# Performance work log

Measured on AMD Instinct MI355X. Metric: run time of the kernel, lower is better.

## Reference

```python
import jax, jax.numpy as jnp
import numpy as np

MIN_CURV = 1e-06
MIN_NORM = 1e-15

def _norm(x):
    return jnp.clip(jnp.linalg.norm(x, axis=-1, keepdims=True), MIN_NORM, None)

def lorentz_expmap0(v, c):
    sqrt_c = jnp.sqrt(c)
    vn = _norm(v)
    x0 = jnp.cosh(sqrt_c * vn) / sqrt_c
    xs = jnp.sinh(sqrt_c * vn) * v / (sqrt_c * vn)
    return jnp.concatenate([x0, xs], axis=-1)

def lorentz_logmap0(x, c):
    sqrt_c = jnp.sqrt(c)
    x0 = x[..., 0:1]
    xs = x[..., 1:]
    xs_norm = _norm(xs)
    theta = jnp.arccosh(jnp.clip(sqrt_c * x0, 1.0 + 1e-07, None))
    return theta / (sqrt_c * xs_norm) * xs

def lorentz_project(x, c):
    spatial = x[..., 1:]
    sq = jnp.sum(spatial * spatial, axis=-1, keepdims=True)
    x0 = jnp.clip(jnp.sqrt(sq + 1.0 / c), MIN_NORM, None)
    return jnp.concatenate([x0, spatial], axis=-1)

def givens_rotation(x, angles):
    x0 = x[..., 0:1]
    xs = x[..., 1:]
    cos_a = jnp.cos(angles)
    sin_a = jnp.sin(angles)
    xe = xs[..., 0::2]
    xo = xs[..., 1::2]
    ne = cos_a * xe - sin_a * xo
    no = sin_a * xe + cos_a * xo
    xr = jnp.stack([ne, no], axis=-1).reshape(xs.shape)
    return jnp.concatenate([x0, xr], axis=-1)

def setup_inputs() -> dict:
    key = jax.random.key(0)
    ks = jax.random.split(key, 16)
    N_NODE, E, B = 50000, 500000, 64
    IN_DIM, OUT_DIM, ATTN_DIM, N_REL = 128, 128, 128, 200
    N_EMB = 2 * N_REL + 1  # 401
    hidden = jax.random.normal(ks[0], (N_NODE, IN_DIM), dtype=jnp.float32)
    q_sub = jax.random.randint(ks[1], (B,), 0, N_NODE)
    q_rel = jax.random.randint(ks[2], (B,), 0, N_EMB)
    r_idx = jax.random.randint(ks[3], (E,), 0, B)
    rel = jax.random.randint(ks[4], (E,), 0, N_EMB)
    sub = jax.random.randint(ks[5], (E,), 0, N_NODE)
    obj = jax.random.randint(ks[6], (E,), 0, N_NODE)
    zeros = jnp.zeros((E,), dtype=jnp.int32)
    edges = jnp.stack([r_idx, zeros, rel, zeros, sub, obj], axis=1)
    rela_embed = jax.random.normal(ks[7], (N_EMB, IN_DIM), dtype=jnp.float32)
    rel_angles = jax.random.uniform(ks[8], (N_EMB, IN_DIM // 2), minval=-0.1, maxval=0.1, dtype=jnp.float32)
    curvature = jnp.array(1.0, dtype=jnp.float32)
    Ws_w = jax.random.normal(ks[9], (ATTN_DIM, IN_DIM), dtype=jnp.float32) * 0.05
    Wr_w = jax.random.normal(ks[10], (ATTN_DIM, IN_DIM), dtype=jnp.float32) * 0.05
    Wqr_w = jax.random.normal(ks[11], (ATTN_DIM, IN_DIM), dtype=jnp.float32) * 0.05
    Wqr_b = jax.random.normal(ks[12], (ATTN_DIM,), dtype=jnp.float32) * 0.05
    Wattn_w = jax.random.normal(ks[13], (1, ATTN_DIM), dtype=jnp.float32) * 0.05
    Wh_w = jax.random.normal(ks[14], (OUT_DIM, IN_DIM), dtype=jnp.float32) * 0.05
    return {"hidden": hidden, "rela_embed": rela_embed, "rel_angles": rel_angles,
            "curvature": curvature, "Ws_w": Ws_w, "Wr_w": Wr_w, "Wqr_w": Wqr_w,
            "Wqr_b": Wqr_b, "Wattn_w": Wattn_w, "Wh_w": Wh_w,
            "q_sub": q_sub, "q_rel": q_rel, "edges": edges,
            "n_node": N_NODE, "old_nodes_new_idx": jnp.arange(N_NODE)}

def reference(hidden, rela_embed, rel_angles, curvature, Ws_w, Wr_w, Wqr_w, Wqr_b,
              Wattn_w, Wh_w, q_sub, q_rel, edges, n_node, old_nodes_new_idx):
    sub = edges[:, 4]
    rel = edges[:, 2]
    obj = edges[:, 5]
    r_idx = edges[:, 0]
    hs = hidden[sub]                      # [E, in_dim]
    hr = rela_embed[rel]                  # [E, in_dim]
    h_qr = rela_embed[q_rel][r_idx]       # [E, in_dim]
    pre = jax.nn.relu(hs @ Ws_w.T + hr @ Wr_w.T + h_qr @ Wqr_w.T + Wqr_b)
    alpha = jax.nn.sigmoid(pre @ Wattn_w.T)  # [E, 1]
    c = jnp.clip(curvature, MIN_CURV, None)
    mess_tangent = hs + hr
    mess_L = lorentz_expmap0(mess_tangent, c)          # [E, in_dim+1]
    mess_L = givens_rotation(mess_L, rel_angles[rel])
    mess2 = lorentz_logmap0(mess_L, c)                 # [E, in_dim]
    message = mess2 * alpha
    message_agg = jax.ops.segment_sum(message, obj, num_segments=n_node)
    a = message_agg @ Wh_w.T                           # [n_node, out_dim]
    a_L = lorentz_expmap0(a, c)
    # act is identity; project back to hyperboloid and log-map
    a_L = lorentz_project(jnp.concatenate([a_L[..., 0:1], a_L[..., 1:]], axis=-1), c)
    hidden_new = lorentz_logmap0(a_L, c)
    return hidden_new
```

## Files before the change

kernel.cpp:

```cpp
#include <hip/hip_runtime.h>
#include <math.h>

#define D 128
#define CAP 36

typedef _Float16 f16x8 __attribute__((ext_vector_type(8)));
typedef _Float16 f16x4 __attribute__((ext_vector_type(4)));
typedef _Float16 f16x2 __attribute__((ext_vector_type(2)));
typedef float    f32x4 __attribute__((ext_vector_type(4)));

union H8 { f16x8 v; f16x4 q[2]; f16x2 p[4]; _Float16 f[8]; };
union H4 { f16x4 v; f16x2 p[2]; _Float16 f[4]; };

__device__ __forceinline__ float fdot2f(f16x2 a, f16x2 b, float c){
  return __builtin_amdgcn_fdot2(a, b, c, false);
}
__device__ __forceinline__ f16x2 relu2(f16x2 x){
  f16x2 r;
  r[0] = x[0] > (_Float16)0 ? x[0] : (_Float16)0;
  r[1] = x[1] > (_Float16)0 ? x[1] : (_Float16)0;
  return r;
}
__device__ __forceinline__ float rsum32(float v){
  v += __shfl_xor(v, 16);
  v += __shfl_xor(v, 8);
  v += __shfl_xor(v, 4);
  v += __shfl_xor(v, 2);
  v += __shfl_xor(v, 1);
  return v;
}

__global__ void k_cvt_small(const float* __restrict__ rela,
                            const float* __restrict__ rel_angles,
                            const float* __restrict__ Ws, const float* __restrict__ Wr,
                            const float* __restrict__ Wh,
                            _Float16* __restrict__ rela16, _Float16* __restrict__ relhq,
                            _Float16* __restrict__ relcs, _Float16* __restrict__ Ws16,
                            _Float16* __restrict__ Wr16, _Float16* __restrict__ Wh16,
                            int* __restrict__ cnt, int NEMB, int NN){
  int idx = blockIdx.x*blockDim.x + threadIdx.x;
  int T1 = NEMB*32;
  if (idx < T1){
    int r = idx >> 5, l = idx & 31;
    float4 hv = *(const float4*)(rela + (size_t)r*D + l*4);
    f16x4 h = { (_Float16)hv.x, (_Float16)hv.y, (_Float16)hv.z, (_Float16)hv.w };
    *(f16x4*)(rela16 + (size_t)r*D + l*4) = h;
    *(f16x4*)(relhq  + (size_t)r*256 + l*8) = h;
    float2 an = *(const float2*)(rel_angles + (size_t)r*(D/2) + l*2);
    float c0 = cosf(an.x), s0 = sinf(an.x);
    float c1 = cosf(an.y), s1 = sinf(an.y);
    H8 cs;
    cs.f[0]=(_Float16)c0; cs.f[1]=(_Float16)(-s0); cs.f[2]=(_Float16)s0; cs.f[3]=(_Float16)c0;
    cs.f[4]=(_Float16)c1; cs.f[5]=(_Float16)(-s1); cs.f[6]=(_Float16)s1; cs.f[7]=(_Float16)c1;
    *(f16x8*)(relcs + (size_t)r*256 + l*8) = cs.v;
    return;
  }
  int j = idx - T1;
  if (j < 3*D*D/4){
    const float* src = (j < 4096) ? Ws : (j < 8192) ? Wr : Wh;
    _Float16*    dst = (j < 4096) ? Ws16 : (j < 8192) ? Wr16 : Wh16;
    int o = (j & 4095)*4;
    float4 v = *(const float4*)(src + o);
    f16x4 h = { (_Float16)v.x, (_Float16)v.y, (_Float16)v.z, (_Float16)v.w };
    *(f16x4*)(dst + o) = h;
    return;
  }
  j -= 3*D*D/4;
  if (j < NN) cnt[j] = 0;
}

__global__ __launch_bounds__(128) void k_prep2(const float* __restrict__ rela,
                                               const float* __restrict__ Wqr,
                                               const float* __restrict__ Wqr_b,
                                               const int* __restrict__ q_rel,
                                               _Float16* __restrict__ hqw16){
  int b = blockIdx.x; int t = threadIdx.x;
  __shared__ float emb[D];
  emb[t] = rela[(size_t)q_rel[b]*D + t];
  __syncthreads();
  float acc = Wqr_b[t];
  #pragma unroll 8
  for (int k=0;k<D;k++) acc += emb[k]*Wqr[t*D + k];
  int p = ((t & 15) << 3) + (t >> 4);
  hqw16[b*D + p] = (_Float16)acc;
}

template<int OUTMODE>
__global__ __launch_bounds__(256) void k_hgemm(const _Float16* __restrict__ A,
                                               const _Float16* __restrict__ W,
                                               void* __restrict__ Out, int M){
  int wave = threadIdx.x >> 6;
  int lane = threadIdx.x & 63;
  int quad = lane >> 4;
  int lo   = lane & 15;
  int m0 = blockIdx.x*64 + wave*16;
  int arow = min(m0 + lo, M-1);
  f32x4 acc[8];
  #pragma unroll
  for (int nt=0;nt<8;nt++) acc[nt] = (f32x4){0.f,0.f,0.f,0.f};
  #pragma unroll
  for (int kt=0;kt<4;kt++){
    f16x8 a = *(const f16x8*)(A + (size_t)arow*D + kt*32 + quad*8);
    #pragma unroll
    for (int nt=0;nt<8;nt++){
      f16x8 b = *(const f16x8*)(W + (size_t)(nt*16 + lo)*D + kt*32 + quad*8);
      acc[nt] = __builtin_amdgcn_mfma_f32_16x16x32_f16(a, b, acc[nt], 0, 0, 0);
    }
  }
  int r0 = m0 + quad*4;
  if (OUTMODE == 0){
    float* O = (float*)Out;
    #pragma unroll
    for (int nt=0;nt<8;nt++){
      int c = nt*16 + lo;
      #pragma unroll
      for (int i=0;i<4;i++){
        int r = r0 + i;
        if (r < M) O[(size_t)r*D + c] = acc[nt][i];
      }
    }
  } else {
    _Float16* O = (_Float16*)Out;
    #pragma unroll
    for (int i=0;i<4;i++){
      int r = r0 + i;
      if (r < M){
        H4 s1, s2;
        #pragma unroll
        for (int nt=0;nt<4;nt++){
          s1.f[nt] = (_Float16)acc[nt][i];
          s2.f[nt] = (_Float16)acc[nt+4][i];
        }
        *(f16x4*)(O + (size_t)r*256 + lo*16 + 4)  = s1.v;
        *(f16x4*)(O + (size_t)r*256 + lo*16 + 12) = s2.v;
      }
    }
  }
}

__global__ __launch_bounds__(256) void k_hgemm_h(const float* __restrict__ A,
                                                 const _Float16* __restrict__ W,
                                                 _Float16* __restrict__ O, int M){
  int wave = threadIdx.x >> 6;
  int lane = threadIdx.x & 63;
  int quad = lane >> 4;
  int lo   = lane & 15;
  int m0 = blockIdx.x*64 + wave*16;
  int arow = min(m0 + lo, M-1);
  f32x4 acc[8];
  #pragma unroll
  for (int nt=0;nt<8;nt++) acc[nt] = (f32x4){0.f,0.f,0.f,0.f};
  H8 hpack[4];
  #pragma unroll
  for (int kt=0;kt<4;kt++){
    float4 a0 = *(const float4*)(A + (size_t)arow*D + kt*32 + quad*8);
    float4 a1 = *(const float4*)(A + (size_t)arow*D + kt*32 + quad*8 + 4);
    H8 a;
    a.f[0]=(_Float16)a0.x; a.f[1]=(_Float16)a0.y; a.f[2]=(_Float16)a0.z; a.f[3]=(_Float16)a0.w;
    a.f[4]=(_Float16)a1.x; a.f[5]=(_Float16)a1.y; a.f[6]=(_Float16)a1.z; a.f[7]=(_Float16)a1.w;
    hpack[kt] = a;
    #pragma unroll
    for (int nt=0;nt<8;nt++){
      f16x8 b = *(const f16x8*)(W + (size_t)(nt*16 + lo)*D + kt*32 + quad*8);
      acc[nt] = __builtin_amdgcn_mfma_f32_16x16x32_f16(a.v, b, acc[nt], 0, 0, 0);
    }
  }
  if (m0 + lo < M){
    #pragma unroll
    for (int kt=0;kt<4;kt++){
      int g = kt*8 + quad*2;
      *(f16x4*)(O + (size_t)arow*256 + g*8)     = hpack[kt].q[0];
      *(f16x4*)(O + (size_t)arow*256 + (g+1)*8) = hpack[kt].q[1];
    }
  }
  int r0 = m0 + quad*4;
  #pragma unroll
  for (int i=0;i<4;i++){
    int r = r0 + i;
    if (r < M){
      H4 s1, s2;
      #pragma unroll
      for (int nt=0;nt<4;nt++){
        s1.f[nt] = (_Float16)acc[nt][i];
        s2.f[nt] = (_Float16)acc[nt+4][i];
      }
      *(f16x4*)(O + (size_t)r*256 + lo*16 + 4)  = s1.v;
      *(f16x4*)(O + (size_t)r*256 + lo*16 + 12) = s2.v;
    }
  }
}

__global__ void k_scatter(const int* __restrict__ edges, int* __restrict__ cnt,
                          int* __restrict__ bucket, int E){
  int base = (blockIdx.x*blockDim.x + threadIdx.x)*2;
  #pragma unroll
  for (int u=0; u<2; u++){
    int e = base + u;
    if (e < E){
      const int* er = edges + (size_t)e*6;
      int ri = er[0], rel = er[2], sub = er[4], obj = er[5];
      int key = sub | (rel << 17) | (ri << 26);
      int pos = atomicAdd(cnt + obj, 1);
      if (pos < CAP) bucket[obj*CAP + pos] = key;
    }
  }
}

__device__ __forceinline__ void edge_op(int key,
    const _Float16* __restrict__ hw16, const _Float16* __restrict__ relcs,
    const _Float16* __restrict__ relhq, const _Float16* __restrict__ hqw16,
    unsigned lh8, unsigned lh4, f16x2 wa01, f16x2 wa23,
    float& ax, float& ay, float& az, float& aw){
  unsigned sub = key & 0x1FFFF, rel = ((unsigned)key >> 17) & 0x1FF, ri = (unsigned)key >> 26;
  H8 hw; hw.v = *(const f16x8*)(hw16  + (sub << 8) + lh8);
  H8 cs; cs.v = *(const f16x8*)(relcs + (rel << 8) + lh8);
  H8 hq; hq.v = *(const f16x8*)(relhq + (rel << 8) + lh8);
  H4 qw; qw.v = *(const f16x4*)(hqw16 + (ri  << 7) + lh4);
  f16x2 t01 = relu2(hw.p[2] + hq.p[2] + qw.p[0]);
  f16x2 t23 = relu2(hw.p[3] + hq.p[3] + qw.p[1]);
  float s = fdot2f(t01, wa01, fdot2f(t23, wa23, 0.f));
  s = rsum32(s);
  float al = __builtin_amdgcn_rcpf(1.f + __expf(-s));
  f16x2 v01 = hw.p[0] + hq.p[0];
  f16x2 v23 = hw.p[1] + hq.p[1];
  ax += al * fdot2f(cs.p[0], v01, 0.f);
  ay += al * fdot2f(cs.p[1], v01, 0.f);
  az += al * fdot2f(cs.p[2], v23, 0.f);
  aw += al * fdot2f(cs.p[3], v23, 0.f);
}

__global__ __launch_bounds__(256) void k_aggregate(
    const _Float16* __restrict__ hw16, const _Float16* __restrict__ relcs,
    const _Float16* __restrict__ relhq, const _Float16* __restrict__ hqw16,
    const float* __restrict__ Wattn, const int* __restrict__ cnt,
    const int* __restrict__ bucket, _Float16* __restrict__ agg16, int NN){
  int t = threadIdx.x;
  int wave = t >> 6;
  int half = (t >> 5) & 1;
  int l = t & 31;
  int n = blockIdx.x*4 + wave;
  if (n >= NN) return;
  unsigned lh8 = (unsigned)l*8, lh4 = (unsigned)l*4;
  unsigned p0 = (unsigned)l*4;
  float w0 = Wattn[(((p0+0)&7)<<4) + ((p0+0)>>3)];
  float w1 = Wattn[(((p0+1)&7)<<4) + ((p0+1)>>3)];
  float w2 = Wattn[(((p0+2)&7)<<4) + ((p0+2)>>3)];
  float w3 = Wattn[(((p0+3)&7)<<4) + ((p0+3)>>3)];
  f16x2 wa01 = { (_Float16)w0, (_Float16)w1 };
  f16x2 wa23 = { (_Float16)w2, (_Float16)w3 };

  int deg = min(cnt[n], CAP);
  const int* bk = bucket + n*CAP;
  float ax=0.f, ay=0.f, az=0.f, aw=0.f;

  for (int i = half*4; i < deg; i += 8){
    int m = deg - i;
    if (m >= 4){
      int4 q = *(const int4*)(bk + i);
      edge_op(q.x, hw16, relcs, relhq, hqw16, lh8, lh4, wa01, wa23, ax, ay, az, aw);
      edge_op(q.y, hw16, relcs, relhq, hqw16, lh8, lh4, wa01, wa23, ax, ay, az, aw);
      edge_op(q.z, hw16, relcs, relhq, hqw16, lh8, lh4, wa01, wa23, ax, ay, az, aw);
      edge_op(q.w, hw16, relcs, relhq, hqw16, lh8, lh4, wa01, wa23, ax, ay, az, aw);
    } else {
      for (int j=0;j<m;j++)
        edge_op(bk[i+j], hw16, relcs, relhq, hqw16, lh8, lh4, wa01, wa23, ax, ay, az, aw);
    }
  }
  ax += __shfl_xor(ax, 32);
  ay += __shfl_xor(ay, 32);
  az += __shfl_xor(az, 32);
  aw += __shfl_xor(aw, 32);
  if (half == 0){
    f16x4 o = { (_Float16)ax, (_Float16)ay, (_Float16)az, (_Float16)aw };
    *(f16x4*)(agg16 + ((size_t)n << 7) + lh4) = o;
  }
}

extern "C" void kernel_launch(void* const* d_in, const int* in_sizes, int n_in,
                              void* d_out, int out_size, void* d_ws, size_t ws_size,
                              hipStream_t stream){
  const float* hidden     = (const float*)d_in[0];
  const float* rela       = (const float*)d_in[1];
  const float* rel_angles = (const float*)d_in[2];
  const float* Ws         = (const float*)d_in[4];
  const float* Wr         = (const float*)d_in[5];
  const float* Wqr        = (const float*)d_in[6];
  const float* Wqr_b      = (const float*)d_in[7];
  const float* Wattn      = (const float*)d_in[8];
  const float* Wh         = (const float*)d_in[9];
  const int*   q_rel      = (const int*)d_in[11];
  const int*   edges      = (const int*)d_in[12];

  int NN   = in_sizes[0] / D;
  int NEMB = in_sizes[1] / D;
  int B    = in_sizes[11];
  int E    = in_sizes[12] / 6;

  char* p = (char*)d_ws;
  auto alloc = [&](size_t bytes)->char*{
    char* r = p; p += (bytes + 255) & ~(size_t)255; return r;
  };
  _Float16* hw16   = (_Float16*)alloc((size_t)NN*256*2);
  _Float16* agg16  = (_Float16*)alloc((size_t)NN*D*2);
  _Float16* rela16 = (_Float16*)alloc((size_t)NEMB*D*2);
  _Float16* relhq  = (_Float16*)alloc((size_t)NEMB*256*2);
  _Float16* relcs  = (_Float16*)alloc((size_t)NEMB*256*2);
  _Float16* hqw16  = (_Float16*)alloc((size_t)B*D*2);
  _Float16* Ws16   = (_Float16*)alloc((size_t)D*D*2);
  _Float16* Wr16   = (_Float16*)alloc((size_t)D*D*2);
  _Float16* Wh16   = (_Float16*)alloc((size_t)D*D*2);
  int*      cnt    = (int*)alloc((size_t)NN*4);
  int*      bucket = (int*)alloc((size_t)NN*CAP*4);

  int smallN = NEMB*32 + 3*D*D/4 + NN;
  k_cvt_small<<<(smallN+255)/256, 256, 0, stream>>>(rela, rel_angles, Ws, Wr, Wh,
                                                    rela16, relhq, relcs,
                                                    Ws16, Wr16, Wh16, cnt, NEMB, NN);
  k_prep2<<<B, 128, 0, stream>>>(rela, Wqr, Wqr_b, q_rel, hqw16);
  k_hgemm<1><<<(NEMB+63)/64, 256, 0, stream>>>(rela16, Wr16, relhq, NEMB);
  k_hgemm_h<<<(NN+63)/64, 256, 0, stream>>>(hidden, Ws16, hw16, NN);
  k_scatter<<<(E/2+255)/256, 256, 0, stream>>>(edges, cnt, bucket, E);
  k_aggregate<<<(NN+3)/4, 256, 0, stream>>>(hw16, relcs, relhq, hqw16,
                                            Wattn, cnt, bucket, agg16, NN);
  k_hgemm<0><<<(NN+63)/64, 256, 0, stream>>>(agg16, Wh16, d_out, NN);
}
```

Baseline: 259.3 us.

## Remap aggregate to 8 edges per wave with wider per-lane feature tiles

The aggregate kernel now has each wave process 8 edges at once, with 8 lanes per edge and each lane covering 16 features. Previously it walked edges sequentially with 32 lanes per edge. To match, the packed fp16 tables (relhq, relcs, hw16, hqw16) are relaid so each lane reads contiguous 32-element chunks with 16-byte loads, and the GEMM epilogues write 16-byte vectors. The attention reduction drops from a 5-step shuffle to 3 steps, in exchange for a 48-shuffle final cross-group reduction and more registers per lane. The scatter kernel also reads edge rows as int4 vectors.

After: 270.7 us. 1.04x slower.

```diff
diff --git a/kernel.cpp b/kernel.cpp
--- a/kernel.cpp
+++ b/kernel.cpp
@@ -10,7 +10,7 @@
 typedef float    f32x4 __attribute__((ext_vector_type(4)));
 
 union H8 { f16x8 v; f16x4 q[2]; f16x2 p[4]; _Float16 f[8]; };
-union H4 { f16x4 v; f16x2 p[2]; _Float16 f[4]; };
+
 
 __device__ __forceinline__ float fdot2f(f16x2 a, f16x2 b, float c){
   return __builtin_amdgcn_fdot2(a, b, c, false);
@@ -20,14 +20,6 @@
   r[0] = x[0] > (_Float16)0 ? x[0] : (_Float16)0;
   r[1] = x[1] > (_Float16)0 ? x[1] : (_Float16)0;
   return r;
-}
-__device__ __forceinline__ float rsum32(float v){
-  v += __shfl_xor(v, 16);
-  v += __shfl_xor(v, 8);
-  v += __shfl_xor(v, 4);
-  v += __shfl_xor(v, 2);
-  v += __shfl_xor(v, 1);
-  return v;
 }
 
 __global__ void k_cvt_small(const float* __restrict__ rela,
@@ -45,14 +37,14 @@
     float4 hv = *(const float4*)(rela + (size_t)r*D + l*4);
     f16x4 h = { (_Float16)hv.x, (_Float16)hv.y, (_Float16)hv.z, (_Float16)hv.w };
     *(f16x4*)(rela16 + (size_t)r*D + l*4) = h;
-    *(f16x4*)(relhq  + (size_t)r*256 + l*8) = h;
+    *(f16x4*)(relhq + (size_t)r*256 + (l>>2)*32 + (l&3)*4) = h;
     float2 an = *(const float2*)(rel_angles + (size_t)r*(D/2) + l*2);
     float c0 = cosf(an.x), s0 = sinf(an.x);
     float c1 = cosf(an.y), s1 = sinf(an.y);
     H8 cs;
     cs.f[0]=(_Float16)c0; cs.f[1]=(_Float16)(-s0); cs.f[2]=(_Float16)s0; cs.f[3]=(_Float16)c0;
     cs.f[4]=(_Float16)c1; cs.f[5]=(_Float16)(-s1); cs.f[6]=(_Float16)s1; cs.f[7]=(_Float16)c1;
-    *(f16x8*)(relcs + (size_t)r*256 + l*8) = cs.v;
+    *(f16x8*)(relcs + (size_t)r*256 + (l>>2)*32 + (l&3)*8) = cs.v;
     return;
   }
   int j = idx - T1;
@@ -81,7 +73,7 @@
   float acc = Wqr_b[t];
   #pragma unroll 8
   for (int k=0;k<D;k++) acc += emb[k]*Wqr[t*D + k];
-  int p = ((t & 15) << 3) + (t >> 4);
+  int p = (t&7)*16 + (t&8) + (t>>4);
   hqw16[b*D + p] = (_Float16)acc;
 }
 
@@ -121,18 +113,15 @@
     }
   } else {
     _Float16* O = (_Float16*)Out;
+    int wbase = (lo&7)*32 + 16 + (lo&8);
     #pragma unroll
     for (int i=0;i<4;i++){
       int r = r0 + i;
       if (r < M){
-        H4 s1, s2;
+        H8 s;
         #pragma unroll
-        for (int nt=0;nt<4;nt++){
-          s1.f[nt] = (_Float16)acc[nt][i];
-          s2.f[nt] = (_Float16)acc[nt+4][i];
-        }
-        *(f16x4*)(O + (size_t)r*256 + lo*16 + 4)  = s1.v;
-        *(f16x4*)(O + (size_t)r*256 + lo*16 + 12) = s2.v;
+        for (int nt=0;nt<8;nt++) s.f[nt] = (_Float16)acc[nt][i];
+        *(f16x8*)(O + (size_t)r*256 + wbase) = s.v;
       }
     }
   }
@@ -168,65 +157,40 @@
   if (m0 + lo < M){
     #pragma unroll
     for (int kt=0;kt<4;kt++){
-      int g = kt*8 + quad*2;
-      *(f16x4*)(O + (size_t)arow*256 + g*8)     = hpack[kt].q[0];
-      *(f16x4*)(O + (size_t)arow*256 + (g+1)*8) = hpack[kt].q[1];
+      int base = (kt*2 + (quad>>1))*32 + (quad&1)*8;
+      *(f16x8*)(O + (size_t)arow*256 + base) = hpack[kt].v;
     }
   }
   int r0 = m0 + quad*4;
+  int wbase = (lo&7)*32 + 16 + (lo&8);
   #pragma unroll
   for (int i=0;i<4;i++){
     int r = r0 + i;
     if (r < M){
-      H4 s1, s2;
+      H8 s;
       #pragma unroll
-      for (int nt=0;nt<4;nt++){
-        s1.f[nt] = (_Float16)acc[nt][i];
-        s2.f[nt] = (_Float16)acc[nt+4][i];
-      }
-      *(f16x4*)(O + (size_t)r*256 + lo*16 + 4)  = s1.v;
-      *(f16x4*)(O + (size_t)r*256 + lo*16 + 12) = s2.v;
+      for (int nt=0;nt<8;nt++) s.f[nt] = (_Float16)acc[nt][i];
+      *(f16x8*)(O + (size_t)r*256 + wbase) = s.v;
     }
   }
 }
 
 __global__ void k_scatter(const int* __restrict__ edges, int* __restrict__ cnt,
                           int* __restrict__ bucket, int E){
-  int base = (blockIdx.x*blockDim.x + threadIdx.x)*2;
-  #pragma unroll
-  for (int u=0; u<2; u++){
-    int e = base + u;
-    if (e < E){
-      const int* er = edges + (size_t)e*6;
-      int ri = er[0], rel = er[2], sub = er[4], obj = er[5];
-      int key = sub | (rel << 17) | (ri << 26);
-      int pos = atomicAdd(cnt + obj, 1);
-      if (pos < CAP) bucket[obj*CAP + pos] = key;
-    }
-  }
-}
-
-__device__ __forceinline__ void edge_op(int key,
-    const _Float16* __restrict__ hw16, const _Float16* __restrict__ relcs,
-    const _Float16* __restrict__ relhq, const _Float16* __restrict__ hqw16,
-    unsigned lh8, unsigned lh4, f16x2 wa01, f16x2 wa23,
-    float& ax, float& ay, float& az, float& aw){
-  unsigned sub = key & 0x1FFFF, rel = ((unsigned)key >> 17) & 0x1FF, ri = (unsigned)key >> 26;
-  H8 hw; hw.v = *(const f16x8*)(hw16  + (sub << 8) + lh8);
-  H8 cs; cs.v = *(const f16x8*)(relcs + (rel << 8) + lh8);
-  H8 hq; hq.v = *(const f16x8*)(relhq + (rel << 8) + lh8);
-  H4 qw; qw.v = *(const f16x4*)(hqw16 + (ri  << 7) + lh4);
-  f16x2 t01 = relu2(hw.p[2] + hq.p[2] + qw.p[0]);
-  f16x2 t23 = relu2(hw.p[3] + hq.p[3] + qw.p[1]);
-  float s = fdot2f(t01, wa01, fdot2f(t23, wa23, 0.f));
-  s = rsum32(s);
-  float al = __builtin_amdgcn_rcpf(1.f + __expf(-s));
-  f16x2 v01 = hw.p[0] + hq.p[0];
-  f16x2 v23 = hw.p[1] + hq.p[1];
-  ax += al * fdot2f(cs.p[0], v01, 0.f);
-  ay += al * fdot2f(cs.p[1], v01, 0.f);
-  az += al * fdot2f(cs.p[2], v23, 0.f);
-  aw += al * fdot2f(cs.p[3], v23, 0.f);
+  int e0 = (blockIdx.x*blockDim.x + threadIdx.x)*2;
+  if (e0 >= E) return;
+  const int4* q = (const int4*)(edges + (size_t)e0*6);
+  int4 q0 = q[0], q1 = q[1], q2 = q[2];
+  {
+    int key = q1.x | (q0.z << 17) | (q0.x << 26);
+    int pos = atomicAdd(cnt + q1.y, 1);
+    if (pos < CAP) bucket[q1.y*CAP + pos] = key;
+  }
+  if (e0 + 1 < E){
+    int key = q2.z | (q2.x << 17) | (q1.z << 26);
+    int pos = atomicAdd(cnt + q2.w, 1);
+    if (pos < CAP) bucket[q2.w*CAP + pos] = key;
+  }
 }
 
 __global__ __launch_bounds__(256) void k_aggregate(
@@ -235,44 +199,80 @@
     const float* __restrict__ Wattn, const int* __restrict__ cnt,
     const int* __restrict__ bucket, _Float16* __restrict__ agg16, int NN){
   int t = threadIdx.x;
-  int wave = t >> 6;
-  int half = (t >> 5) & 1;
-  int l = t & 31;
+  int wave = t >> 6, lane = t & 63;
+  int g = lane >> 3, j = lane & 7;
   int n = blockIdx.x*4 + wave;
   if (n >= NN) return;
-  unsigned lh8 = (unsigned)l*8, lh4 = (unsigned)l*4;
-  unsigned p0 = (unsigned)l*4;
-  float w0 = Wattn[(((p0+0)&7)<<4) + ((p0+0)>>3)];
-  float w1 = Wattn[(((p0+1)&7)<<4) + ((p0+1)>>3)];
-  float w2 = Wattn[(((p0+2)&7)<<4) + ((p0+2)>>3)];
-  float w3 = Wattn[(((p0+3)&7)<<4) + ((p0+3)>>3)];
-  f16x2 wa01 = { (_Float16)w0, (_Float16)w1 };
-  f16x2 wa23 = { (_Float16)w2, (_Float16)w3 };
+
+  f16x2 wa[8];
+  #pragma unroll
+  for (int q2=0;q2<8;q2++){
+    int qa = q2*2, qb = q2*2+1;
+    float w0 = Wattn[j + (qa&8) + 16*(qa&7)];
+    float w1 = Wattn[j + (qb&8) + 16*(qb&7)];
+    wa[q2] = (f16x2){ (_Float16)w0, (_Float16)w1 };
+  }
 
   int deg = min(cnt[n], CAP);
   const int* bk = bucket + n*CAP;
-  float ax=0.f, ay=0.f, az=0.f, aw=0.f;
-
-  for (int i = half*4; i < deg; i += 8){
-    int m = deg - i;
-    if (m >= 4){
-      int4 q = *(const int4*)(bk + i);
-      edge_op(q.x, hw16, relcs, relhq, hqw16, lh8, lh4, wa01, wa23, ax, ay, az, aw);
-      edge_op(q.y, hw16, relcs, relhq, hqw16, lh8, lh4, wa01, wa23, ax, ay, az, aw);
-      edge_op(q.z, hw16, relcs, relhq, hqw16, lh8, lh4, wa01, wa23, ax, ay, az, aw);
-      edge_op(q.w, hw16, relcs, relhq, hqw16, lh8, lh4, wa01, wa23, ax, ay, az, aw);
-    } else {
-      for (int j=0;j<m;j++)
-        edge_op(bk[i+j], hw16, relcs, relhq, hqw16, lh8, lh4, wa01, wa23, ax, ay, az, aw);
-    }
-  }
-  ax += __shfl_xor(ax, 32);
-  ay += __shfl_xor(ay, 32);
-  az += __shfl_xor(az, 32);
-  aw += __shfl_xor(aw, 32);
-  if (half == 0){
-    f16x4 o = { (_Float16)ax, (_Float16)ay, (_Float16)az, (_Float16)aw };
-    *(f16x4*)(agg16 + ((size_t)n << 7) + lh4) = o;
+  float acc[16];
+  #pragma unroll
+  for (int k=0;k<16;k++) acc[k] = 0.f;
+  unsigned jo32 = (unsigned)j*32, jo16 = (unsigned)j*16;
+
+  for (int i = 0; i < deg; i += 8){
+    int idx = i + g;
+    bool valid = idx < deg;
+    int key = bk[valid ? idx : 0];
+    unsigned sub = key & 0x1FFFF, rel = ((unsigned)key >> 17) & 0x1FF, ri = (unsigned)key >> 26;
+    const _Float16* hwp = hw16  + ((size_t)sub << 8) + jo32;
+    const _Float16* csp = relcs + ((size_t)rel << 8) + jo32;
+    const _Float16* hqp = relhq + ((size_t)rel << 8) + jo32;
+    const _Float16* qwp = hqw16 + ((size_t)ri  << 7) + jo16;
+
+    H8 h0, h1, w0, w1, c0, c1, c2, c3, rh0, rh1, rw0, rw1, qa, qb;
+    h0.v  = *(const f16x8*)(hwp);       h1.v  = *(const f16x8*)(hwp + 8);
+    w0.v  = *(const f16x8*)(hwp + 16);  w1.v  = *(const f16x8*)(hwp + 24);
+    c0.v  = *(const f16x8*)(csp);       c1.v  = *(const f16x8*)(csp + 8);
+    c2.v  = *(const f16x8*)(csp + 16);  c3.v  = *(const f16x8*)(csp + 24);
+    rh0.v = *(const f16x8*)(hqp);       rh1.v = *(const f16x8*)(hqp + 8);
+    rw0.v = *(const f16x8*)(hqp + 16);  rw1.v = *(const f16x8*)(hqp + 24);
+    qa.v  = *(const f16x8*)(qwp);       qb.v  = *(const f16x8*)(qwp + 8);
+
+    float s = 0.f;
+    #pragma unroll
+    for (int p=0;p<4;p++){
+      s = fdot2f(relu2(w0.p[p] + rw0.p[p] + qa.p[p]), wa[p],   s);
+      s = fdot2f(relu2(w1.p[p] + rw1.p[p] + qb.p[p]), wa[p+4], s);
+    }
+    s += __shfl_xor(s, 1);
+    s += __shfl_xor(s, 2);
+    s += __shfl_xor(s, 4);
+    float al = valid ? __builtin_amdgcn_rcpf(1.f + __expf(-s)) : 0.f;
+
+    f16x2 v;
+    v = h0.p[0] + rh0.p[0]; acc[0] += al*fdot2f(c0.p[0], v, 0.f); acc[1] += al*fdot2f(c0.p[1], v, 0.f);
+    v = h0.p[1] + rh0.p[1]; acc[2] += al*fdot2f(c0.p[2], v, 0.f); acc[3] += al*fdot2f(c0.p[3], v, 0.f);
+    v = h0.p[2] + rh0.p[2]; acc[4] += al*fdot2f(c1.p[0], v, 0.f); acc[5] += al*fdot2f(c1.p[1], v, 0.f);
+    v = h0.p[3] + rh0.p[3]; acc[6] += al*fdot2f(c1.p[2], v, 0.f); acc[7] += al*fdot2f(c1.p[3], v, 0.f);
+    v = h1.p[0] + rh1.p[0]; acc[8] += al*fdot2f(c2.p[0], v, 0.f); acc[9] += al*fdot2f(c2.p[1], v, 0.f);
+    v = h1.p[1] + rh1.p[1]; acc[10]+= al*fdot2f(c2.p[2], v, 0.f); acc[11]+= al*fdot2f(c2.p[3], v, 0.f);
+    v = h1.p[2] + rh1.p[2]; acc[12]+= al*fdot2f(c3.p[0], v, 0.f); acc[13]+= al*fdot2f(c3.p[1], v, 0.f);
+    v = h1.p[3] + rh1.p[3]; acc[14]+= al*fdot2f(c3.p[2], v, 0.f); acc[15]+= al*fdot2f(c3.p[3], v, 0.f);
+  }
+
+  #pragma unroll
+  for (int k=0;k<16;k++){
+    acc[k] += __shfl_xor(acc[k], 8);
+    acc[k] += __shfl_xor(acc[k], 16);
+    acc[k] += __shfl_xor(acc[k], 32);
+  }
+  if (g == 0){
+    H8 oA, oB;
+    #pragma unroll
+    for (int k=0;k<8;k++){ oA.f[k] = (_Float16)acc[k]; oB.f[k] = (_Float16)acc[8+k]; }
+    *(f16x8*)(agg16 + ((size_t)n << 7) + jo16)     = oA.v;
+    *(f16x8*)(agg16 + ((size_t)n << 7) + jo16 + 8) = oB.v;
   }
 }
 
```

## Merge prep, scatter and GEMM kernels into fewer launches; one node per half-wave

Applied to the files above, without the earlier changes.

Merges the conversion and query-projection kernels into one launch. It also merges the edge scatter, the hidden GEMM and the relation GEMM into a single block-partitioned mega kernel, cutting seven launches to four and letting the independent stages run concurrently. The scatter now reads four edges per thread with vector loads. The aggregate kernel assigns one node per 32-lane half-wave instead of splitting a node's edges across two halves, which drops the cross-half shuffle reduction but gives each lane a longer serial edge loop.

Result: faster. 239.1 us (-7.8%).

```diff
diff --git a/kernel.cpp b/kernel.cpp
--- a/kernel.cpp
+++ b/kernel.cpp
@@ -30,74 +30,10 @@
   return v;
 }
 
-__global__ void k_cvt_small(const float* __restrict__ rela,
-                            const float* __restrict__ rel_angles,
-                            const float* __restrict__ Ws, const float* __restrict__ Wr,
-                            const float* __restrict__ Wh,
-                            _Float16* __restrict__ rela16, _Float16* __restrict__ relhq,
-                            _Float16* __restrict__ relcs, _Float16* __restrict__ Ws16,
-                            _Float16* __restrict__ Wr16, _Float16* __restrict__ Wh16,
-                            int* __restrict__ cnt, int NEMB, int NN){
-  int idx = blockIdx.x*blockDim.x + threadIdx.x;
-  int T1 = NEMB*32;
-  if (idx < T1){
-    int r = idx >> 5, l = idx & 31;
-    float4 hv = *(const float4*)(rela + (size_t)r*D + l*4);
-    f16x4 h = { (_Float16)hv.x, (_Float16)hv.y, (_Float16)hv.z, (_Float16)hv.w };
-    *(f16x4*)(rela16 + (size_t)r*D + l*4) = h;
-    *(f16x4*)(relhq  + (size_t)r*256 + l*8) = h;
-    float2 an = *(const float2*)(rel_angles + (size_t)r*(D/2) + l*2);
-    float c0 = cosf(an.x), s0 = sinf(an.x);
-    float c1 = cosf(an.y), s1 = sinf(an.y);
-    H8 cs;
-    cs.f[0]=(_Float16)c0; cs.f[1]=(_Float16)(-s0); cs.f[2]=(_Float16)s0; cs.f[3]=(_Float16)c0;
-    cs.f[4]=(_Float16)c1; cs.f[5]=(_Float16)(-s1); cs.f[6]=(_Float16)s1; cs.f[7]=(_Float16)c1;
-    *(f16x8*)(relcs + (size_t)r*256 + l*8) = cs.v;
-    return;
-  }
-  int j = idx - T1;
-  if (j < 3*D*D/4){
-    const float* src = (j < 4096) ? Ws : (j < 8192) ? Wr : Wh;
-    _Float16*    dst = (j < 4096) ? Ws16 : (j < 8192) ? Wr16 : Wh16;
-    int o = (j & 4095)*4;
-    float4 v = *(const float4*)(src + o);
-    f16x4 h = { (_Float16)v.x, (_Float16)v.y, (_Float16)v.z, (_Float16)v.w };
-    *(f16x4*)(dst + o) = h;
-    return;
-  }
-  j -= 3*D*D/4;
-  if (j < NN) cnt[j] = 0;
-}
-
-__global__ __launch_bounds__(128) void k_prep2(const float* __restrict__ rela,
-                                               const float* __restrict__ Wqr,
-                                               const float* __restrict__ Wqr_b,
-                                               const int* __restrict__ q_rel,
-                                               _Float16* __restrict__ hqw16){
-  int b = blockIdx.x; int t = threadIdx.x;
-  __shared__ float emb[D];
-  emb[t] = rela[(size_t)q_rel[b]*D + t];
-  __syncthreads();
-  float acc = Wqr_b[t];
-  #pragma unroll 8
-  for (int k=0;k<D;k++) acc += emb[k]*Wqr[t*D + k];
-  int p = ((t & 15) << 3) + (t >> 4);
-  hqw16[b*D + p] = (_Float16)acc;
-}
-
-template<int OUTMODE>
-__global__ __launch_bounds__(256) void k_hgemm(const _Float16* __restrict__ A,
-                                               const _Float16* __restrict__ W,
-                                               void* __restrict__ Out, int M){
-  int wave = threadIdx.x >> 6;
-  int lane = threadIdx.x & 63;
-  int quad = lane >> 4;
-  int lo   = lane & 15;
-  int m0 = blockIdx.x*64 + wave*16;
-  int arow = min(m0 + lo, M-1);
-  f32x4 acc[8];
-  #pragma unroll
-  for (int nt=0;nt<8;nt++) acc[nt] = (f32x4){0.f,0.f,0.f,0.f};
+
+__device__ __forceinline__ void hgemm_core16(const _Float16* __restrict__ A,
+                                             const _Float16* __restrict__ W,
+                                             int arow, f32x4 acc[8], int quad, int lo){
   #pragma unroll
   for (int kt=0;kt<4;kt++){
     f16x8 a = *(const f16x8*)(A + (size_t)arow*D + kt*32 + quad*8);
@@ -107,72 +43,10 @@
       acc[nt] = __builtin_amdgcn_mfma_f32_16x16x32_f16(a, b, acc[nt], 0, 0, 0);
     }
   }
-  int r0 = m0 + quad*4;
-  if (OUTMODE == 0){
-    float* O = (float*)Out;
-    #pragma unroll
-    for (int nt=0;nt<8;nt++){
-      int c = nt*16 + lo;
-      #pragma unroll
-      for (int i=0;i<4;i++){
-        int r = r0 + i;
-        if (r < M) O[(size_t)r*D + c] = acc[nt][i];
-      }
-    }
-  } else {
-    _Float16* O = (_Float16*)Out;
-    #pragma unroll
-    for (int i=0;i<4;i++){
-      int r = r0 + i;
-      if (r < M){
-        H4 s1, s2;
-        #pragma unroll
-        for (int nt=0;nt<4;nt++){
-          s1.f[nt] = (_Float16)acc[nt][i];
-          s2.f[nt] = (_Float16)acc[nt+4][i];
-        }
-        *(f16x4*)(O + (size_t)r*256 + lo*16 + 4)  = s1.v;
-        *(f16x4*)(O + (size_t)r*256 + lo*16 + 12) = s2.v;
-      }
-    }
-  }
-}
-
-__global__ __launch_bounds__(256) void k_hgemm_h(const float* __restrict__ A,
-                                                 const _Float16* __restrict__ W,
-                                                 _Float16* __restrict__ O, int M){
-  int wave = threadIdx.x >> 6;
-  int lane = threadIdx.x & 63;
-  int quad = lane >> 4;
-  int lo   = lane & 15;
-  int m0 = blockIdx.x*64 + wave*16;
-  int arow = min(m0 + lo, M-1);
-  f32x4 acc[8];
-  #pragma unroll
-  for (int nt=0;nt<8;nt++) acc[nt] = (f32x4){0.f,0.f,0.f,0.f};
-  H8 hpack[4];
-  #pragma unroll
-  for (int kt=0;kt<4;kt++){
-    float4 a0 = *(const float4*)(A + (size_t)arow*D + kt*32 + quad*8);
-    float4 a1 = *(const float4*)(A + (size_t)arow*D + kt*32 + quad*8 + 4);
-    H8 a;
-    a.f[0]=(_Float16)a0.x; a.f[1]=(_Float16)a0.y; a.f[2]=(_Float16)a0.z; a.f[3]=(_Float16)a0.w;
-    a.f[4]=(_Float16)a1.x; a.f[5]=(_Float16)a1.y; a.f[6]=(_Float16)a1.z; a.f[7]=(_Float16)a1.w;
-    hpack[kt] = a;
-    #pragma unroll
-    for (int nt=0;nt<8;nt++){
-      f16x8 b = *(const f16x8*)(W + (size_t)(nt*16 + lo)*D + kt*32 + quad*8);
-      acc[nt] = __builtin_amdgcn_mfma_f32_16x16x32_f16(a.v, b, acc[nt], 0, 0, 0);
-    }
-  }
-  if (m0 + lo < M){
-    #pragma unroll
-    for (int kt=0;kt<4;kt++){
-      int g = kt*8 + quad*2;
-      *(f16x4*)(O + (size_t)arow*256 + g*8)     = hpack[kt].q[0];
-      *(f16x4*)(O + (size_t)arow*256 + (g+1)*8) = hpack[kt].q[1];
-    }
-  }
+}
+
+__device__ __forceinline__ void store_wpart(_Float16* __restrict__ O, f32x4 acc[8],
+                                            int m0, int quad, int lo, int M){
   int r0 = m0 + quad*4;
   #pragma unroll
   for (int i=0;i<4;i++){
@@ -190,19 +64,145 @@
   }
 }
 
-__global__ void k_scatter(const int* __restrict__ edges, int* __restrict__ cnt,
-                          int* __restrict__ bucket, int E){
-  int base = (blockIdx.x*blockDim.x + threadIdx.x)*2;
-  #pragma unroll
-  for (int u=0; u<2; u++){
-    int e = base + u;
-    if (e < E){
-      const int* er = edges + (size_t)e*6;
-      int ri = er[0], rel = er[2], sub = er[4], obj = er[5];
-      int key = sub | (rel << 17) | (ri << 26);
-      int pos = atomicAdd(cnt + obj, 1);
-      if (pos < CAP) bucket[obj*CAP + pos] = key;
-    }
+__global__ __launch_bounds__(256) void k_prep(
+    const float* __restrict__ rela, const float* __restrict__ rel_angles,
+    const float* __restrict__ Ws, const float* __restrict__ Wr,
+    const float* __restrict__ Wh, const float* __restrict__ Wqr,
+    const float* __restrict__ Wqr_b, const int* __restrict__ q_rel,
+    _Float16* __restrict__ rela16, _Float16* __restrict__ relhq,
+    _Float16* __restrict__ relcs, _Float16* __restrict__ Ws16,
+    _Float16* __restrict__ Wr16, _Float16* __restrict__ Wh16,
+    _Float16* __restrict__ hqw16, int* __restrict__ cnt,
+    int NEMB, int NN, int PA){
+  __shared__ float emb[D];
+  int b = blockIdx.x;
+  int t = threadIdx.x;
+  if (b < PA){
+    int idx = b*256 + t;
+    int T1 = NEMB*32;
+    if (idx < T1){
+      int r = idx >> 5, l = idx & 31;
+      float4 hv = *(const float4*)(rela + (size_t)r*D + l*4);
+      f16x4 h = { (_Float16)hv.x, (_Float16)hv.y, (_Float16)hv.z, (_Float16)hv.w };
+      *(f16x4*)(rela16 + (size_t)r*D + l*4) = h;
+      *(f16x4*)(relhq  + (size_t)r*256 + l*8) = h;
+      float2 an = *(const float2*)(rel_angles + (size_t)r*(D/2) + l*2);
+      float c0 = cosf(an.x), s0 = sinf(an.x);
+      float c1 = cosf(an.y), s1 = sinf(an.y);
+      H8 cs;
+      cs.f[0]=(_Float16)c0; cs.f[1]=(_Float16)(-s0); cs.f[2]=(_Float16)s0; cs.f[3]=(_Float16)c0;
+      cs.f[4]=(_Float16)c1; cs.f[5]=(_Float16)(-s1); cs.f[6]=(_Float16)s1; cs.f[7]=(_Float16)c1;
+      *(f16x8*)(relcs + (size_t)r*256 + l*8) = cs.v;
+      return;
+    }
+    int j = idx - T1;
+    if (j < 3*D*D/4){
+      const float* src = (j < 4096) ? Ws : (j < 8192) ? Wr : Wh;
+      _Float16*    dst = (j < 4096) ? Ws16 : (j < 8192) ? Wr16 : Wh16;
+      int o = (j & 4095)*4;
+      float4 v = *(const float4*)(src + o);
+      f16x4 h = { (_Float16)v.x, (_Float16)v.y, (_Float16)v.z, (_Float16)v.w };
+      *(f16x4*)(dst + o) = h;
+      return;
+    }
+    j -= 3*D*D/4;
+    if (j < NN) cnt[j] = 0;
+  } else {
+    int bb = b - PA;
+    if (t < D) emb[t] = rela[(size_t)q_rel[bb]*D + t];
+    __syncthreads();
+    if (t < D){
+      float acc = Wqr_b[t];
+      #pragma unroll 8
+      for (int k=0;k<D;k++) acc += emb[k]*Wqr[t*D + k];
+      int p = ((t & 15) << 3) + (t >> 4);
+      hqw16[bb*D + p] = (_Float16)acc;
+    }
+  }
+}
+
+__global__ __launch_bounds__(256) void k_mega(
+    const int* __restrict__ edges, int* __restrict__ cnt, int* __restrict__ bucket,
+    int E, const float* __restrict__ hidden, const _Float16* __restrict__ Ws16,
+    _Float16* __restrict__ hw16, int NN,
+    const _Float16* __restrict__ rela16, const _Float16* __restrict__ Wr16,
+    _Float16* __restrict__ relhq, int NEMB, int SB, int GH){
+  int b = blockIdx.x;
+  if (b < SB){
+    int e0 = (b*256 + threadIdx.x)*4;
+    if (e0 >= E) return;
+    if (e0 + 3 < E){
+      const int4* q = (const int4*)(edges + (size_t)e0*6);
+      int4 q0=q[0], q1=q[1], q2=q[2], q3=q[3], q4=q[4], q5=q[5];
+      int key0 = q1.x | (q0.z << 17) | (q0.x << 26);
+      int key1 = q2.z | (q2.x << 17) | (q1.z << 26);
+      int key2 = q4.x | (q3.z << 17) | (q3.x << 26);
+      int key3 = q5.z | (q5.x << 17) | (q4.z << 26);
+      int p0 = atomicAdd(cnt + q1.y, 1);
+      int p1 = atomicAdd(cnt + q2.w, 1);
+      int p2 = atomicAdd(cnt + q4.y, 1);
+      int p3 = atomicAdd(cnt + q5.w, 1);
+      if (p0 < CAP) bucket[q1.y*CAP + p0] = key0;
+      if (p1 < CAP) bucket[q2.w*CAP + p1] = key1;
+      if (p2 < CAP) bucket[q4.y*CAP + p2] = key2;
+      if (p3 < CAP) bucket[q5.w*CAP + p3] = key3;
+    } else {
+      for (int u=0; u<4; u++){
+        int e = e0 + u;
+        if (e < E){
+          const int* er = edges + (size_t)e*6;
+          int key = er[4] | (er[2] << 17) | (er[0] << 26);
+          int pos = atomicAdd(cnt + er[5], 1);
+          if (pos < CAP) bucket[er[5]*CAP + pos] = key;
+        }
+      }
+    }
+  } else if (b < SB + GH){
+    int bb = b - SB;
+    int wave = threadIdx.x >> 6;
+    int lane = threadIdx.x & 63;
+    int quad = lane >> 4, lo = lane & 15;
+    int m0 = bb*64 + wave*16;
+    int arow = min(m0 + lo, NN-1);
+    f32x4 acc[8];
+    #pragma unroll
+    for (int nt=0;nt<8;nt++) acc[nt] = (f32x4){0.f,0.f,0.f,0.f};
+    H8 hpack[4];
+    #pragma unroll
+    for (int kt=0;kt<4;kt++){
+      float4 a0 = *(const float4*)(hidden + (size_t)arow*D + kt*32 + quad*8);
+      float4 a1 = *(const float4*)(hidden + (size_t)arow*D + kt*32 + quad*8 + 4);
+      H8 a;
+      a.f[0]=(_Float16)a0.x; a.f[1]=(_Float16)a0.y; a.f[2]=(_Float16)a0.z; a.f[3]=(_Float16)a0.w;
+      a.f[4]=(_Float16)a1.x; a.f[5]=(_Float16)a1.y; a.f[6]=(_Float16)a1.z; a.f[7]=(_Float16)a1.w;
+      hpack[kt] = a;
+      #pragma unroll
+      for (int nt=0;nt<8;nt++){
+        f16x8 bb2 = *(const f16x8*)(Ws16 + (size_t)(nt*16 + lo)*D + kt*32 + quad*8);
+        acc[nt] = __builtin_amdgcn_mfma_f32_16x16x32_f16(a.v, bb2, acc[nt], 0, 0, 0);
+      }
+    }
+    if (m0 + lo < NN){
+      #pragma unroll
+      for (int kt=0;kt<4;kt++){
+        int g = kt*8 + quad*2;
+        *(f16x4*)(hw16 + (size_t)arow*256 + g*8)     = hpack[kt].q[0];
+        *(f16x4*)(hw16 + (size_t)arow*256 + (g+1)*8) = hpack[kt].q[1];
+      }
+    }
+    store_wpart(hw16, acc, m0, quad, lo, NN);
+  } else {
+    int bb = b - SB - GH;
+    int wave = threadIdx.x >> 6;
+    int lane = threadIdx.x & 63;
+    int quad = lane >> 4, lo = lane & 15;
+    int m0 = bb*64 + wave*16;
+    int arow = min(m0 + lo, NEMB-1);
+    f32x4 acc[8];
+    #pragma unroll
+    for (int nt=0;nt<8;nt++) acc[nt] = (f32x4){0.f,0.f,0.f,0.f};
+    hgemm_core16(rela16, Wr16, arow, acc, quad, lo);
+    store_wpart(relhq, acc, m0, quad, lo, NEMB);
   }
 }
 
@@ -235,10 +235,8 @@
     const float* __restrict__ Wattn, const int* __restrict__ cnt,
     const int* __restrict__ bucket, _Float16* __restrict__ agg16, int NN){
   int t = threadIdx.x;
-  int wave = t >> 6;
-  int half = (t >> 5) & 1;
-  int l = t & 31;
-  int n = blockIdx.x*4 + wave;
+  int half = t >> 5, l = t & 31;
+  int n = blockIdx.x*8 + half;
   if (n >= NN) return;
   unsigned lh8 = (unsigned)l*8, lh4 = (unsigned)l*4;
   unsigned p0 = (unsigned)l*4;
@@ -253,26 +251,42 @@
   const int* bk = bucket + n*CAP;
   float ax=0.f, ay=0.f, az=0.f, aw=0.f;
 
-  for (int i = half*4; i < deg; i += 8){
-    int m = deg - i;
-    if (m >= 4){
-      int4 q = *(const int4*)(bk + i);
-      edge_op(q.x, hw16, relcs, relhq, hqw16, lh8, lh4, wa01, wa23, ax, ay, az, aw);
-      edge_op(q.y, hw16, relcs, relhq, hqw16, lh8, lh4, wa01, wa23, ax, ay, az, aw);
-      edge_op(q.z, hw16, relcs, relhq, hqw16, lh8, lh4, wa01, wa23, ax, ay, az, aw);
-      edge_op(q.w, hw16, relcs, relhq, hqw16, lh8, lh4, wa01, wa23, ax, ay, az, aw);
-    } else {
-      for (int j=0;j<m;j++)
-        edge_op(bk[i+j], hw16, relcs, relhq, hqw16, lh8, lh4, wa01, wa23, ax, ay, az, aw);
-    }
-  }
-  ax += __shfl_xor(ax, 32);
-  ay += __shfl_xor(ay, 32);
-  az += __shfl_xor(az, 32);
-  aw += __shfl_xor(aw, 32);
-  if (half == 0){
-    f16x4 o = { (_Float16)ax, (_Float16)ay, (_Float16)az, (_Float16)aw };
-    *(f16x4*)(agg16 + ((size_t)n << 7) + lh4) = o;
+  int i = 0;
+  for (; i+4 <= deg; i += 4){
+    int4 q = *(const int4*)(bk + i);
+    edge_op(q.x, hw16, relcs, relhq, hqw16, lh8, lh4, wa01, wa23, ax, ay, az, aw);
+    edge_op(q.y, hw16, relcs, relhq, hqw16, lh8, lh4, wa01, wa23, ax, ay, az, aw);
+    edge_op(q.z, hw16, relcs, relhq, hqw16, lh8, lh4, wa01, wa23, ax, ay, az, aw);
+    edge_op(q.w, hw16, relcs, relhq, hqw16, lh8, lh4, wa01, wa23, ax, ay, az, aw);
+  }
+  for (; i < deg; i++)
+    edge_op(bk[i], hw16, relcs, relhq, hqw16, lh8, lh4, wa01, wa23, ax, ay, az, aw);
+
+  f16x4 o = { (_Float16)ax, (_Float16)ay, (_Float16)az, (_Float16)aw };
+  *(f16x4*)(agg16 + ((size_t)n << 7) + lh4) = o;
+}
+
+__global__ __launch_bounds__(256) void k_hgemm0(const _Float16* __restrict__ A,
+                                                const _Float16* __restrict__ W,
+                                                float* __restrict__ O, int M){
+  int wave = threadIdx.x >> 6;
+  int lane = threadIdx.x & 63;
+  int quad = lane >> 4, lo = lane & 15;
+  int m0 = blockIdx.x*64 + wave*16;
+  int arow = min(m0 + lo, M-1);
+  f32x4 acc[8];
+  #pragma unroll
+  for (int nt=0;nt<8;nt++) acc[nt] = (f32x4){0.f,0.f,0.f,0.f};
+  hgemm_core16(A, W, arow, acc, quad, lo);
+  int r0 = m0 + quad*4;
+  #pragma unroll
+  for (int nt=0;nt<8;nt++){
+    int c = nt*16 + lo;
+    #pragma unroll
+    for (int i=0;i<4;i++){
+      int r = r0 + i;
+      if (r < M) O[(size_t)r*D + c] = acc[nt][i];
+    }
   }
 }
 
@@ -313,14 +327,19 @@
   int*      bucket = (int*)alloc((size_t)NN*CAP*4);
 
   int smallN = NEMB*32 + 3*D*D/4 + NN;
-  k_cvt_small<<<(smallN+255)/256, 256, 0, stream>>>(rela, rel_angles, Ws, Wr, Wh,
-                                                    rela16, relhq, relcs,
-                                                    Ws16, Wr16, Wh16, cnt, NEMB, NN);
-  k_prep2<<<B, 128, 0, stream>>>(rela, Wqr, Wqr_b, q_rel, hqw16);
-  k_hgemm<1><<<(NEMB+63)/64, 256, 0, stream>>>(rela16, Wr16, relhq, NEMB);
-  k_hgemm_h<<<(NN+63)/64, 256, 0, stream>>>(hidden, Ws16, hw16, NN);
-  k_scatter<<<(E/2+255)/256, 256, 0, stream>>>(edges, cnt, bucket, E);
-  k_aggregate<<<(NN+3)/4, 256, 0, stream>>>(hw16, relcs, relhq, hqw16,
+  int PA = (smallN + 255)/256;
+  k_prep<<<PA + B, 256, 0, stream>>>(rela, rel_angles, Ws, Wr, Wh, Wqr, Wqr_b,
+                                     q_rel, rela16, relhq, relcs, Ws16, Wr16,
+                                     Wh16, hqw16, cnt, NEMB, NN, PA);
+
+  int SB = (E + 1023)/1024;
+  int GH = (NN + 63)/64;
+  int G1 = (NEMB + 63)/64;
+  k_mega<<<SB + GH + G1, 256, 0, stream>>>(edges, cnt, bucket, E, hidden, Ws16,
+                                           hw16, NN, rela16, Wr16, relhq, NEMB,
+                                           SB, GH);
+
+  k_aggregate<<<(NN+7)/8, 256, 0, stream>>>(hw16, relcs, relhq, hqw16,
                                             Wattn, cnt, bucket, agg16, NN);
-  k_hgemm<0><<<(NN+63)/64, 256, 0, stream>>>(agg16, Wh16, d_out, NN);
-}
+  k_hgemm0<<<(NN+63)/64, 256, 0, stream>>>(agg16, Wh16, (float*)d_out, NN);
+}
```
